# Kernel tuning notes

Measured on AMD Instinct MI355X. Metric: run time of the kernel, lower is better.

## Reference

```python
import jax, jax.numpy as jnp
import numpy as np

DIM = 1024
N_STATE = 64
T, B = 512, 32


def _xavier(key, shape):
    fan_out, fan_in = shape
    limit = np.sqrt(6.0 / (fan_in + fan_out)).astype(np.float32)
    return jax.random.uniform(key, shape, jnp.float32, -limit, limit)


def setup_inputs() -> dict:
    key = jax.random.key(0)
    ks = jax.random.split(key, 5)
    return {
        "x": jax.random.normal(ks[0], (T, B, DIM), jnp.float32),
        "S": jnp.zeros((B, N_STATE, N_STATE), jnp.float32),
        "W_k": _xavier(ks[1], (N_STATE, DIM)),
        "W_v": _xavier(ks[2], (N_STATE, DIM)),
        "W_q": _xavier(ks[3], (N_STATE, DIM)),
        "W_alpha": _xavier(ks[4], (N_STATE, DIM)),
        "d_alpha": jnp.full((N_STATE,), 0.1, jnp.float32),
        "b_alpha": jnp.full((N_STATE,), 2.0, jnp.float32),
    }


def reference(x, S, W_k, W_v, W_q, W_alpha, d_alpha, b_alpha):
    # Precompute all projections as batched GEMMs: [T,B,n_state]
    k = jnp.einsum("tbd,nd->tbn", x, W_k)
    v = jnp.einsum("tbd,nd->tbn", x, W_v)
    q = jnp.einsum("tbd,nd->tbn", x, W_q)
    ax = jnp.einsum("tbd,nd->tbn", x, W_alpha)

    def step(S, inp):
        k_t, v_t, q_t, ax_t = inp  # each [B, n_state]
        retrieved = jnp.einsum("bij,bj->bi", S, k_t)          # S @ k
        alpha = jax.nn.sigmoid(ax_t + d_alpha * retrieved + b_alpha)
        # S = alpha * S + (1 - alpha) * outer(v, k); alpha gates rows
        S_new = alpha[:, :, None] * S + (1.0 - alpha)[:, :, None] * (
            v_t[:, :, None] * k_t[:, None, :]
        )
        h = jnp.einsum("bij,bj->bi", S_new, q_t)              # S @ q
        out_t = h * jax.nn.silu(h)                             # self-gated output
        return S_new, out_t

    S_final, output = jax.lax.scan(step, S, (k, v, q, ax))
    return output, S_final
```

## Files before the change

### kernel.cpp

```cpp
#include <hip/hip_runtime.h>
#include <hip/hip_bf16.h>

#define T_STEPS 512
#define BATCH 32
#define NST 64
#define DIM 1024

typedef _Float16 f16x8 __attribute__((ext_vector_type(8)));
typedef _Float16 f16x4 __attribute__((ext_vector_type(4)));
typedef float f32x4 __attribute__((ext_vector_type(4)));
typedef float f32x2 __attribute__((ext_vector_type(2)));

__device__ __forceinline__ void gl_lds16(const void* g, void* l) {
  __builtin_amdgcn_global_load_lds(
      (const __attribute__((address_space(1))) void*)g,
      (__attribute__((address_space(3))) void*)l, 16, 0, 0);
}

__global__ __launch_bounds__(256) void wconv(
    const float* __restrict__ Wk, const float* __restrict__ Wv,
    const float* __restrict__ Wq, const float* __restrict__ Wa,
    _Float16* __restrict__ Wc) {
  const int n = blockIdx.x;
  const int g = n >> 6, r = n & 63;
  const float* W = (g == 0) ? Wk : (g == 1) ? Wq : (g == 2) ? Wv : Wa;
  const float sc = (g == 3) ? -1.44269504088896340736f : 1.0f;
  float4 v = *(const float4*)(W + (size_t)r * DIM + threadIdx.x * 4);
  f16x4 h = {(_Float16)(v.x * sc), (_Float16)(v.y * sc), (_Float16)(v.z * sc),
             (_Float16)(v.w * sc)};
  *(f16x4*)(Wc + (size_t)n * DIM + threadIdx.x * 4) = h;
}

__global__ __launch_bounds__(512) void proj_gemm(
    const float* __restrict__ x, const _Float16* __restrict__ Wc,
    float* __restrict__ projf) {
  const int m0 = blockIdx.x * 64;
  const int tid = threadIdx.x;
  const int lane = tid & 63, wv = tid >> 6;
  const int wm = wv >> 2, wn = wv & 3;
  const int fm = lane & 15, fq = lane >> 4;

  __shared__ __align__(16) _Float16 Bl[2][256 * 32];
  __shared__ __align__(16) _Float16 Al[2][64 * 32];

  const int brow = tid >> 2;
  const int bcg = (tid & 3) ^ ((tid >> 3) & 3);
  const _Float16* gB = Wc + (size_t)brow * DIM + bcg * 8;
  const int bdst = tid * 8;

#define STAGE_B(buf, k0)                                          \
  {                                                               \
    _Pragma("unroll") for (int i = 0; i < 2; ++i)                 \
        gl_lds16(gB + (size_t)i * 128 * DIM + (k0),               \
                 &Bl[buf][i * 4096 + bdst]);                      \
  }

  const int arow = tid >> 3;
  const int afc = (tid & 7) * 4;
  const float* gA = x + (size_t)(m0 + arow) * DIM + afc;
  const int awp = arow * 32 + ((((tid >> 1) & 3) ^ ((arow >> 1) & 3)) * 8) +
                  (tid & 1) * 4;

#define LOADX(rr, k0)                          \
  {                                            \
    rr = *(const float4*)(gA + (k0));          \
  }
#define CVT_WRITE_A(buf, rr)                                        \
  {                                                                 \
    f16x4 h = {(_Float16)rr.x, (_Float16)rr.y, (_Float16)rr.z,      \
               (_Float16)rr.w};                                     \
    *(f16x4*)&Al[buf][awp] = h;                                     \
  }

  f32x4 acc[2][4];
#pragma unroll
  for (int mi = 0; mi < 2; ++mi)
#pragma unroll
    for (int ni = 0; ni < 4; ++ni) acc[mi][ni] = (f32x4){0.f, 0.f, 0.f, 0.f};

  const int aswz = (fq ^ ((fm >> 1) & 3)) * 8;
  const int abase = (wm * 32 + fm) * 32 + aswz;
  const int bbase = (wn * 64 + fm) * 32 + aswz;

#define COMPUTE(cb)                                                     \
  {                                                                     \
    f16x8 afr[2], bfr[4];                                               \
    _Pragma("unroll") for (int mi = 0; mi < 2; ++mi)                    \
        afr[mi] = *(const f16x8*)&Al[cb][abase + mi * 16 * 32];         \
    _Pragma("unroll") for (int ni = 0; ni < 4; ++ni)                    \
        bfr[ni] = *(const f16x8*)&Bl[cb][bbase + ni * 16 * 32];         \
    _Pragma("unroll") for (int mi = 0; mi < 2; ++mi)                    \
        _Pragma("unroll") for (int ni = 0; ni < 4; ++ni)                \
            acc[mi][ni] = __builtin_amdgcn_mfma_f32_16x16x32_f16(       \
                afr[mi], bfr[ni], acc[mi][ni], 0, 0, 0);                \
  }

  float4 rE, rO;
  LOADX(rE, 0);
  STAGE_B(0, 0);
  LOADX(rO, 32);
  CVT_WRITE_A(0, rE);
  __syncthreads();

  for (int k2 = 0; k2 < 16; ++k2) {
    STAGE_B(1, (2 * k2 + 1) * 32);
    if (k2 < 15) LOADX(rE, (2 * k2 + 2) * 32);
    CVT_WRITE_A(1, rO);
    COMPUTE(0);
    __syncthreads();
    if (k2 < 15) {
      STAGE_B(0, (2 * k2 + 2) * 32);
      LOADX(rO, (2 * k2 + 3) * 32);
      CVT_WRITE_A(0, rE);
    }
    COMPUTE(1);
    __syncthreads();
  }
#undef STAGE_B
#undef LOADX
#undef CVT_WRITE_A
#undef COMPUTE

#pragma unroll
  for (int mi = 0; mi < 2; ++mi)
#pragma unroll
    for (int ni = 0; ni < 4; ++ni) {
      const int gcol = wn * 64 + ni * 16 + fm;
      const int pcol = gcol < 128 ? gcol
                     : (gcol < 192 ? 128 + 2 * (gcol - 128) : 129 + 2 * (gcol - 192));
#pragma unroll
      for (int r = 0; r < 4; ++r) {
        const int grow = m0 + wm * 32 + mi * 16 + fq * 4 + r;
        projf[(size_t)grow * 256 + pcol] = acc[mi][ni][r];
      }
    }
}

__device__ __forceinline__ float red16(float x) {
  int v = __builtin_amdgcn_update_dpp(0, __float_as_int(x), 0xB1, 0xF, 0xF, true);
  x += __int_as_float(v);
  v = __builtin_amdgcn_update_dpp(0, __float_as_int(x), 0x4E, 0xF, 0xF, true);
  x += __int_as_float(v);
  v = __builtin_amdgcn_update_dpp(0, __float_as_int(x), 0x124, 0xF, 0xF, true);
  x += __int_as_float(v);
  v = __builtin_amdgcn_update_dpp(0, __float_as_int(x), 0x128, 0xF, 0xF, true);
  x += __int_as_float(v);
  return x;
}

__global__ __launch_bounds__(256, 1) void scan_kernel(
    const float* __restrict__ projf, const float* __restrict__ S0,
    const float* __restrict__ d_alpha, const float* __restrict__ b_alpha,
    float* __restrict__ out, float* __restrict__ Sout) {
  const int b = blockIdx.x >> 2;
  const int rg = blockIdx.x & 3;
  const int tid = threadIdx.x;
  const int c = tid & 15;
  const int lr = tid >> 4;
  const int r = rg * 16 + lr;
  const int j0 = c * 4;

  __shared__ __align__(16) float lbuf[2 * 2048];
  __shared__ __align__(16) float hbuf[8 * 16];

  constexpr float NL2E = -1.44269504088896340736f;
  f32x2 s01, s23;
  {
    float4 v = *(const float4*)(S0 + ((size_t)b * NST + r) * NST + j0);
    s01 = (f32x2){v.x, v.y}; s23 = (f32x2){v.z, v.w};
  }
  const float da2 = d_alpha[r] * NL2E;
  const float ba2 = b_alpha[r] * NL2E;

  const float* gp = projf + (size_t)b * 256;
  const int lidx = (tid >> 5) * 256 + (tid & 31) * 8;
#define GADDR(ch) (gp + (size_t)((ch) * 8 + (tid >> 5)) * (BATCH * 256) + (tid & 31) * 8)

  float4 rA0, rA1;
  rA0 = *(const float4*)GADDR(0); rA1 = *(const float4*)(GADDR(0) + 4);
  *(float4*)(lbuf + lidx) = rA0; *(float4*)(lbuf + lidx + 4) = rA1;
  rA0 = *(const float4*)GADDR(1); rA1 = *(const float4*)(GADDR(1) + 4);
  *(float4*)(lbuf + 2048 + lidx) = rA0; *(float4*)(lbuf + 2048 + lidx + 4) = rA1;
  rA0 = *(const float4*)GADDR(2); rA1 = *(const float4*)(GADDR(2) + 4);
  __syncthreads();

  f32x2 k01[2], k23[2], q01[2], q23[2], va[2];
#define PREF(tn)                                                            \
  {                                                                         \
    const int pp = (tn) & 1;                                                \
    const float* Pn = lbuf + (((tn) >> 3) & 1) * 2048 + ((tn) & 7) * 256;   \
    float4 kk = *(const float4*)(Pn + j0);                                  \
    float4 qq = *(const float4*)(Pn + 64 + j0);                             \
    k01[pp] = (f32x2){kk.x, kk.y}; k23[pp] = (f32x2){kk.z, kk.w};           \
    q01[pp] = (f32x2){qq.x, qq.y}; q23[pp] = (f32x2){qq.z, qq.w};           \
    float2 vv = *(const float2*)(Pn + 128 + 2 * r);                         \
    va[pp] = (f32x2){vv.x, vv.y};                                           \
  }

  PREF(0);
  for (int ch = 0; ch < 64; ++ch) {
#pragma unroll
    for (int si = 0; si < 8; ++si) {
      const int t = ch * 8 + si;
      const int p = t & 1;
      if (t + 1 < T_STEPS) PREF(t + 1);

      f32x2 pa = s01 * k01[p] + s23 * k23[p];
      const float rr = red16(pa[0] + pa[1]);

      float z2 = fmaf(da2, rr, va[p][1] + ba2);
      z2 = fminf(fmaxf(z2, -43.3f), 43.3f);
      const float e = __builtin_amdgcn_exp2f(z2);
      const float al = __builtin_amdgcn_rcpf(1.f + e);
      const float cc = (e * va[p][0]) * al;

      const f32x2 al2 = {al, al}, cc2 = {cc, cc};
      s01 = al2 * s01 + cc2 * k01[p];
      s23 = al2 * s23 + cc2 * k23[p];

      f32x2 hh = s01 * q01[p] + s23 * q23[p];
      const float h = red16(hh[0] + hh[1]);
      if (c == 0) hbuf[si * 16 + lr] = h;
    }
    __syncthreads();
    if (ch + 2 < 64) {
      *(float4*)(lbuf + (ch & 1) * 2048 + lidx) = rA0;
      *(float4*)(lbuf + (ch & 1) * 2048 + lidx + 4) = rA1;
    }
    if (tid < 64) {
      const int tl = tid >> 3;
      const int pr = (tid & 7) * 2;
      float2 hv = *(const float2*)(hbuf + tl * 16 + pr);
      const float e0 = __builtin_amdgcn_exp2f(hv.x * NL2E);
      const float e1 = __builtin_amdgcn_exp2f(hv.y * NL2E);
      float2 y;
      y.x = (hv.x * hv.x) * __builtin_amdgcn_rcpf(1.f + e0);
      y.y = (hv.y * hv.y) * __builtin_amdgcn_rcpf(1.f + e1);
      *(float2*)(out + ((size_t)(ch * 8 + tl) * BATCH + b) * NST + rg * 16 + pr) = y;
    }
    if (ch + 3 < 64) {
      rA0 = *(const float4*)GADDR(ch + 3);
      rA1 = *(const float4*)(GADDR(ch + 3) + 4);
    }
    __syncthreads();
  }
#undef PREF
#undef GADDR

  float4 o = {s01[0], s01[1], s23[0], s23[1]};
  *(float4*)(Sout + ((size_t)b * NST + r) * NST + j0) = o;
}

extern "C" void kernel_launch(void* const* d_in, const int* in_sizes, int n_in,
                              void* d_out, int out_size, void* d_ws, size_t ws_size,
                              hipStream_t stream) {
  const float* x  = (const float*)d_in[0];
  const float* S0 = (const float*)d_in[1];
  const float* Wk = (const float*)d_in[2];
  const float* Wv = (const float*)d_in[3];
  const float* Wq = (const float*)d_in[4];
  const float* Wa = (const float*)d_in[5];
  const float* da = (const float*)d_in[6];
  const float* ba = (const float*)d_in[7];

  float* out  = (float*)d_out;
  float* Sout = out + (size_t)T_STEPS * BATCH * NST;
  float* projf = (float*)d_ws;
  _Float16* Wc = (_Float16*)((char*)d_ws + (size_t)16384 * 256 * 4);

  wconv<<<256, 256, 0, stream>>>(Wk, Wv, Wq, Wa, Wc);
  proj_gemm<<<256, 512, 0, stream>>>(x, Wc, projf);
  scan_kernel<<<4 * BATCH, 256, 0, stream>>>(projf, S0, da, ba, out, Sout);
}
```

Baseline: 218.2 us.

## Split scan into producer and consumer warps to pipeline the output reduction

Doubles the scan block to 512 threads. The first 256 threads run the serial state recurrence and compute alpha and the update coefficient; the second 256 keep a replica of the state, apply the same updates one chunk behind, and compute the h reduction and gated output. This takes the second cross-lane reduction off the critical serial path, at the cost of duplicated state-update work, more LDS buffering (four chunk buffers plus an alpha/cc exchange) and per-chunk block barriers. It also swaps the clamp for fmed3 and writes outputs directly from the consumer threads.

After: 210.6 us. 3.5% less time.

```diff
diff --git a/kernel.cpp b/kernel.cpp
--- a/kernel.cpp
+++ b/kernel.cpp
@@ -148,20 +148,22 @@
   return x;
 }
 
-__global__ __launch_bounds__(256, 1) void scan_kernel(
+__global__ __launch_bounds__(512, 1) void scan_kernel(
     const float* __restrict__ projf, const float* __restrict__ S0,
     const float* __restrict__ d_alpha, const float* __restrict__ b_alpha,
     float* __restrict__ out, float* __restrict__ Sout) {
   const int b = blockIdx.x >> 2;
   const int rg = blockIdx.x & 3;
   const int tid = threadIdx.x;
-  const int c = tid & 15;
-  const int lr = tid >> 4;
+  const bool prod = tid < 256;
+  const int ptid = tid & 255;
+  const int c = ptid & 15;
+  const int lr = ptid >> 4;
   const int r = rg * 16 + lr;
   const int j0 = c * 4;
 
-  __shared__ __align__(16) float lbuf[2 * 2048];
-  __shared__ __align__(16) float hbuf[8 * 16];
+  __shared__ __align__(16) float lbuf[4][2048];
+  __shared__ __align__(16) float2 alcc[2][8][16];
 
   constexpr float NL2E = -1.44269504088896340736f;
   f32x2 s01, s23;
@@ -172,83 +174,102 @@
   const float da2 = d_alpha[r] * NL2E;
   const float ba2 = b_alpha[r] * NL2E;
 
+  const int sstep = tid >> 6;
+  const int soff = (tid & 63) * 4;
+  const int lidx = sstep * 256 + soff;
   const float* gp = projf + (size_t)b * 256;
-  const int lidx = (tid >> 5) * 256 + (tid & 31) * 8;
-#define GADDR(ch) (gp + (size_t)((ch) * 8 + (tid >> 5)) * (BATCH * 256) + (tid & 31) * 8)
-
-  float4 rA0, rA1;
-  rA0 = *(const float4*)GADDR(0); rA1 = *(const float4*)(GADDR(0) + 4);
-  *(float4*)(lbuf + lidx) = rA0; *(float4*)(lbuf + lidx + 4) = rA1;
-  rA0 = *(const float4*)GADDR(1); rA1 = *(const float4*)(GADDR(1) + 4);
-  *(float4*)(lbuf + 2048 + lidx) = rA0; *(float4*)(lbuf + 2048 + lidx + 4) = rA1;
-  rA0 = *(const float4*)GADDR(2); rA1 = *(const float4*)(GADDR(2) + 4);
+#define GADDR(ch) (gp + (size_t)((ch) * 8 + sstep) * (BATCH * 256) + soff)
+
+  float4 rA;
+  rA = *(const float4*)GADDR(0); *(float4*)&lbuf[0][lidx] = rA;
+  rA = *(const float4*)GADDR(1); *(float4*)&lbuf[1][lidx] = rA;
+  rA = *(const float4*)GADDR(2);
   __syncthreads();
 
-  f32x2 k01[2], k23[2], q01[2], q23[2], va[2];
-#define PREF(tn)                                                            \
-  {                                                                         \
-    const int pp = (tn) & 1;                                                \
-    const float* Pn = lbuf + (((tn) >> 3) & 1) * 2048 + ((tn) & 7) * 256;   \
-    float4 kk = *(const float4*)(Pn + j0);                                  \
-    float4 qq = *(const float4*)(Pn + 64 + j0);                             \
-    k01[pp] = (f32x2){kk.x, kk.y}; k23[pp] = (f32x2){kk.z, kk.w};           \
-    q01[pp] = (f32x2){qq.x, qq.y}; q23[pp] = (f32x2){qq.z, qq.w};           \
-    float2 vv = *(const float2*)(Pn + 128 + 2 * r);                         \
-    va[pp] = (f32x2){vv.x, vv.y};                                           \
-  }
-
-  PREF(0);
-  for (int ch = 0; ch < 64; ++ch) {
-#pragma unroll
-    for (int si = 0; si < 8; ++si) {
-      const int t = ch * 8 + si;
-      const int p = t & 1;
-      if (t + 1 < T_STEPS) PREF(t + 1);
-
-      f32x2 pa = s01 * k01[p] + s23 * k23[p];
-      const float rr = red16(pa[0] + pa[1]);
-
-      float z2 = fmaf(da2, rr, va[p][1] + ba2);
-      z2 = fminf(fmaxf(z2, -43.3f), 43.3f);
-      const float e = __builtin_amdgcn_exp2f(z2);
-      const float al = __builtin_amdgcn_rcpf(1.f + e);
-      const float cc = (e * va[p][0]) * al;
-
-      const f32x2 al2 = {al, al}, cc2 = {cc, cc};
-      s01 = al2 * s01 + cc2 * k01[p];
-      s23 = al2 * s23 + cc2 * k23[p];
-
-      f32x2 hh = s01 * q01[p] + s23 * q23[p];
-      const float h = red16(hh[0] + hh[1]);
-      if (c == 0) hbuf[si * 16 + lr] = h;
+  f32x2 k01[2], k23[2], q01[2], q23[2], vaf[2];
+#define PREFP(tn)                                                        \
+  {                                                                      \
+    const int pp = (tn) & 1;                                             \
+    const float* Pn = &lbuf[((tn) >> 3) & 3][((tn) & 7) * 256];          \
+    float4 kk = *(const float4*)(Pn + j0);                               \
+    k01[pp] = (f32x2){kk.x, kk.y}; k23[pp] = (f32x2){kk.z, kk.w};        \
+    float2 vv = *(const float2*)(Pn + 128 + 2 * r);                      \
+    vaf[pp] = (f32x2){vv.x, vv.y};                                       \
+  }
+#define PREFC(tn)                                                        \
+  {                                                                      \
+    const int pp = (tn) & 1;                                             \
+    const float* Pn = &lbuf[((tn) >> 3) & 3][((tn) & 7) * 256];          \
+    float4 kk = *(const float4*)(Pn + j0);                               \
+    k01[pp] = (f32x2){kk.x, kk.y}; k23[pp] = (f32x2){kk.z, kk.w};        \
+    float4 qq = *(const float4*)(Pn + 64 + j0);                          \
+    q01[pp] = (f32x2){qq.x, qq.y}; q23[pp] = (f32x2){qq.z, qq.w};        \
+  }
+
+  if (prod) { PREFP(0); } else { PREFC(0); }
+
+  for (int ch = 0; ch <= 64; ++ch) {
+    if (prod) {
+      if (ch < 64) {
+#pragma unroll
+        for (int si = 0; si < 8; ++si) {
+          const int t = ch * 8 + si;
+          const int p = si & 1;
+          if (t + 1 < T_STEPS) PREFP(t + 1);
+
+          f32x2 pa = s01 * k01[p] + s23 * k23[p];
+          const float rr = red16(pa[0] + pa[1]);
+
+          float z2 = fmaf(da2, rr, vaf[p][1] + ba2);
+          z2 = __builtin_amdgcn_fmed3f(z2, -43.3f, 43.3f);
+          const float e = __builtin_amdgcn_exp2f(z2);
+          const float al = __builtin_amdgcn_rcpf(1.f + e);
+          const float cc = (e * vaf[p][0]) * al;
+
+          const f32x2 al2 = {al, al}, cc2 = {cc, cc};
+          s01 = al2 * s01 + cc2 * k01[p];
+          s23 = al2 * s23 + cc2 * k23[p];
+
+          if (c == 0) alcc[ch & 1][si][lr] = make_float2(al, cc);
+        }
+      }
+    } else {
+      if (ch >= 1) {
+        const int pch = ch - 1;
+#pragma unroll
+        for (int si = 0; si < 8; ++si) {
+          const int t = pch * 8 + si;
+          const int p = si & 1;
+          if (t + 1 < T_STEPS) PREFC(t + 1);
+
+          float2 ac = alcc[pch & 1][si][lr];
+          const f32x2 al2 = {ac.x, ac.x}, cc2 = {ac.y, ac.y};
+          s01 = al2 * s01 + cc2 * k01[p];
+          s23 = al2 * s23 + cc2 * k23[p];
+
+          f32x2 hh = s01 * q01[p] + s23 * q23[p];
+          const float h = red16(hh[0] + hh[1]);
+          if (c == 0) {
+            const float sg =
+                __builtin_amdgcn_rcpf(1.f + __builtin_amdgcn_exp2f(h * NL2E));
+            out[((size_t)t * BATCH + b) * NST + r] = (h * h) * sg;
+          }
+        }
+      }
     }
     __syncthreads();
-    if (ch + 2 < 64) {
-      *(float4*)(lbuf + (ch & 1) * 2048 + lidx) = rA0;
-      *(float4*)(lbuf + (ch & 1) * 2048 + lidx + 4) = rA1;
-    }
-    if (tid < 64) {
-      const int tl = tid >> 3;
-      const int pr = (tid & 7) * 2;
-      float2 hv = *(const float2*)(hbuf + tl * 16 + pr);
-      const float e0 = __builtin_amdgcn_exp2f(hv.x * NL2E);
-      const float e1 = __builtin_amdgcn_exp2f(hv.y * NL2E);
-      float2 y;
-      y.x = (hv.x * hv.x) * __builtin_amdgcn_rcpf(1.f + e0);
-      y.y = (hv.y * hv.y) * __builtin_amdgcn_rcpf(1.f + e1);
-      *(float2*)(out + ((size_t)(ch * 8 + tl) * BATCH + b) * NST + rg * 16 + pr) = y;
-    }
-    if (ch + 3 < 64) {
-      rA0 = *(const float4*)GADDR(ch + 3);
-      rA1 = *(const float4*)(GADDR(ch + 3) + 4);
-    }
-    __syncthreads();
-  }
-#undef PREF
+    if (ch + 2 < 64) *(float4*)&lbuf[(ch + 2) & 3][lidx] = rA;
+    if (ch + 3 < 64) rA = *(const float4*)GADDR(ch + 3);
+    __syncthreads();
+  }
+#undef PREFP
+#undef PREFC
 #undef GADDR
 
-  float4 o = {s01[0], s01[1], s23[0], s23[1]};
-  *(float4*)(Sout + ((size_t)b * NST + r) * NST + j0) = o;
+  if (!prod) {
+    float4 o = {s01[0], s01[1], s23[0], s23[1]};
+    *(float4*)(Sout + ((size_t)b * NST + r) * NST + j0) = o;
+  }
 }
 
 extern "C" void kernel_launch(void* const* d_in, const int* in_sizes, int n_in,
@@ -270,5 +291,5 @@
 
   wconv<<<256, 256, 0, stream>>>(Wk, Wv, Wq, Wa, Wc);
   proj_gemm<<<256, 512, 0, stream>>>(x, Wc, projf);
-  scan_kernel<<<4 * BATCH, 256, 0, stream>>>(projf, S0, da, ba, out, Sout);
-}
+  scan_kernel<<<4 * BATCH, 512, 0, stream>>>(projf, S0, da, ba, out, Sout);
+}
```
